# Kernel optimization log

Hardware: AMD Instinct MI355X
Metric: run time of the kernel (lower is better)

## Reference

```python
import jax, jax.numpy as jnp
import numpy as np

EPS = 1e-7
N, L, BATCH = 512, 2, 128
N_IPF = 10


def setup_inputs() -> dict:
    key = jax.random.key(0)
    k1, k2, k3, k4 = jax.random.split(key, 4)
    return {
        "x": jax.random.randint(k1, (BATCH, N), 0, L, dtype=jnp.int32),
        "W": jax.random.normal(k2, (N, N), dtype=jnp.float32),
        "V_compress": jax.random.normal(k3, (N, L), dtype=jnp.float32),
        "E_compress": jax.random.normal(k4, (N, N, L, L), dtype=jnp.float32),
    }


def _moat_forward(W, V_compress, E_compress, x):
    n, l = V_compress.shape
    # marginals / joints
    V = jax.nn.softmax(V_compress, axis=1)              # (n, l)
    E = jnp.exp(E_compress)                              # (n, n, l, l)
    E = E / E.sum(axis=(-2, -1), keepdims=True)

    # 10-step Sinkhorn / IPF projection onto marginals V
    A_b = V[:, None, :, None]                            # (n, 1, l, 1)
    B_b = V[None, :, None, :]                            # (1, n, 1, l)
    for _ in range(N_IPF):
        row_marg = E.sum(axis=3, keepdims=True) + EPS    # (n, n, l, 1)
        col_marg = E.sum(axis=2, keepdims=True) + EPS    # (n, n, 1, l)
        E = E * (A_b / row_marg)
        E = E * (B_b / col_marg)
        E = E / (E.sum(axis=(-2, -1), keepdims=True) + EPS)

    # zero the diagonal (i == j) pairwise joints, clamp
    E = E * (1.0 - jnp.eye(n, dtype=E.dtype))[:, :, None, None]
    E = jnp.clip(E, 0.0, 1.0)

    # symmetric edge-weight matrix from strictly-lower-triangular sigmoid(W)
    Wm = jax.nn.sigmoid(W)
    Wm = jnp.tril(Wm, k=-1)
    Wm = Wm.T + Wm                                       # (n, n), zero diag
    L_0 = -Wm + jnp.diag(Wm.sum(axis=1))                 # graph Laplacian

    idx = jnp.arange(n)
    # Pr[b, i] = V[i, x[b, i]]
    Pr = V[idx[None, :], x]                              # (batch, n)
    # P[b, i, j] = E[i, j, x[b, i], x[b, j]]
    P = E[idx[None, :, None], idx[None, None, :], x[:, :, None], x[:, None, :]]  # (batch, n, n)
    P = P / (Pr[:, :, None] * Pr[:, None, :])

    WP = Wm[None, :, :] * P                              # (batch, n, n)
    Lb = -WP + jax.vmap(jnp.diag)(WP.sum(axis=2))        # batched Laplacian

    # matrix-tree theorem: logdet of the (n-1, n-1) principal minor
    _, logdet_L = jnp.linalg.slogdet(Lb[:, 1:, 1:])
    _, logdet_L0 = jnp.linalg.slogdet(L_0[1:, 1:])
    return jnp.log(Pr).sum(axis=1) + logdet_L - logdet_L0  # (batch,)


def reference(x, W, V_compress, E_compress):
    return _moat_forward(W, V_compress, E_compress, x)
```

## Files before the change

### kernel.cpp

```cpp
#include <hip/hip_runtime.h>
#include <hip/hip_bf16.h>
#include <math.h>

#define NDIM 512
#define NB   128
#define NMAT 129
#define EPSF 1e-7f
#define MS  ((size_t)262144)
#define LTS ((size_t)32768)
#define PSTR ((size_t)524288)

#define OFF_E   ((size_t)0)
#define OFF_WM  ((size_t)1048576)
#define OFF_V   ((size_t)(OFF_WM + 262144))
#define OFF_IPR ((size_t)(OFF_V + 1024))
#define OFF_LPR ((size_t)(OFF_IPR + 65536))
#define OFF_LD  ((size_t)(OFF_LPR + 128))
#define OFF_LT  ((size_t)1377792)
#define OFF_MAT ((size_t)(OFF_LT + (size_t)NMAT*LTS))

__device__ __forceinline__ float rdlane(float v, int l) {
  return __uint_as_float((unsigned)__builtin_amdgcn_readlane((int)__float_as_uint(v), l));
}

__global__ __launch_bounds__(256) void k_V(const float* __restrict__ Vc, float* __restrict__ V) {
  int i = blockIdx.x * 256 + threadIdx.x;
  if (i < NDIM) {
    float v0 = Vc[2*i], v1 = Vc[2*i+1];
    float mx = fmaxf(v0, v1);
    float e0 = expf(v0 - mx), e1 = expf(v1 - mx);
    float s = e0 + e1;
    V[2*i]   = e0 / s;
    V[2*i+1] = e1 / s;
  }
}

__global__ __launch_bounds__(256) void k_Wm(const float* __restrict__ W, float* __restrict__ Wm) {
  int idx = blockIdx.x * 256 + threadIdx.x;
  int i = idx >> 9, j = idx & 511;
  float v = 0.f;
  if (i > j)      v = 1.f / (1.f + expf(-W[i*NDIM + j]));
  else if (i < j) v = 1.f / (1.f + expf(-W[j*NDIM + i]));
  Wm[idx] = v;
}

__global__ __launch_bounds__(256) void k_E(const float* __restrict__ Ec, const float* __restrict__ V,
                                           float* __restrict__ E2) {
  int idx = blockIdx.x * 256 + threadIdx.x;
  int i = idx >> 9, j = idx & 511;
  float4 ec = reinterpret_cast<const float4*>(Ec)[idx];
  float e00 = expf(ec.x), e01 = expf(ec.y), e10 = expf(ec.z), e11 = expf(ec.w);
  float s = e00 + e01 + e10 + e11;
  float inv = 1.f / s;
  e00 *= inv; e01 *= inv; e10 *= inv; e11 *= inv;
  float A0 = V[2*i], A1 = V[2*i+1];
  float B0 = V[2*j], B1 = V[2*j+1];
  for (int t = 0; t < 10; ++t) {
    float rm0 = e00 + e01 + EPSF, rm1 = e10 + e11 + EPSF;
    float cm0 = e00 + e10 + EPSF, cm1 = e01 + e11 + EPSF;
    float f0 = A0 / rm0, f1 = A1 / rm1;
    e00 *= f0; e01 *= f0; e10 *= f1; e11 *= f1;
    float g0 = B0 / cm0, g1 = B1 / cm1;
    e00 *= g0; e10 *= g0; e01 *= g1; e11 *= g1;
    float ss = e00 + e01 + e10 + e11 + EPSF;
    float iv = 1.f / ss;
    e00 *= iv; e01 *= iv; e10 *= iv; e11 *= iv;
  }
  if (i == j) { e00 = 0.f; e01 = 0.f; e10 = 0.f; e11 = 0.f; }
  e00 = fminf(fmaxf(e00, 0.f), 1.f);
  e01 = fminf(fmaxf(e01, 0.f), 1.f);
  e10 = fminf(fmaxf(e10, 0.f), 1.f);
  e11 = fminf(fmaxf(e11, 0.f), 1.f);
  reinterpret_cast<float2*>(E2)[idx]               = make_float2(e00, e01);
  reinterpret_cast<float2*>(E2 + PSTR)[idx]        = make_float2(e10, e11);
}

__global__ __launch_bounds__(256) void k_Pr(const int* __restrict__ x, const float* __restrict__ V,
                                            float* __restrict__ invPr, float* __restrict__ logPr) {
  const int b = blockIdx.x;
  const int tid = threadIdx.x;
  float acc = 0.f;
  for (int ii = tid; ii < NDIM; ii += 256) {
    const int xv = x[b*NDIM + ii];
    const float p = V[2*ii + xv];
    invPr[b*NDIM + ii] = 1.f / p;
    acc += logf(p);
  }
  for (int off = 32; off > 0; off >>= 1) acc += __shfl_down(acc, off, 64);
  __shared__ float sw[4];
  if ((tid & 63) == 0) sw[tid >> 6] = acc;
  __syncthreads();
  if (tid == 0) logPr[b] = sw[0] + sw[1] + sw[2] + sw[3];
}

__global__ __launch_bounds__(512) void k_build(const int* __restrict__ x, const float* __restrict__ E2,
                                               const float* __restrict__ Wm, const float* __restrict__ invPr,
                                               float* __restrict__ Mall) {
  const int b = blockIdx.x;
  const int i = blockIdx.y*8 + (threadIdx.x >> 6);
  const int lane = threadIdx.x & 63;
  const int j0 = lane << 3;

  const float4 w0 = *(const float4*)(Wm + (size_t)i*NDIM + j0);
  const float4 w1 = *(const float4*)(Wm + (size_t)i*NDIM + j0 + 4);
  float wp[8];
  if (b < NB) {
    const int   xi   = x[b*NDIM + i];
    const float ipri = invPr[b*NDIM + i];
    const int4  xa = *(const int4*)(x + b*NDIM + j0);
    const int4  xb = *(const int4*)(x + b*NDIM + j0 + 4);
    const float4 pa = *(const float4*)(invPr + b*NDIM + j0);
    const float4 pb = *(const float4*)(invPr + b*NDIM + j0 + 4);
    const float* pl = E2 + (size_t)xi*PSTR + ((size_t)i*NDIM + j0)*2;
    const float4 ea = *(const float4*)(pl);
    const float4 eb = *(const float4*)(pl + 4);
    const float4 ec = *(const float4*)(pl + 8);
    const float4 ed = *(const float4*)(pl + 12);
    wp[0] = w0.x * (xa.x ? ea.y : ea.x) * pa.x;
    wp[1] = w0.y * (xa.y ? ea.w : ea.z) * pa.y;
    wp[2] = w0.z * (xa.z ? eb.y : eb.x) * pa.z;
    wp[3] = w0.w * (xa.w ? eb.w : eb.z) * pa.w;
    wp[4] = w1.x * (xb.x ? ec.y : ec.x) * pb.x;
    wp[5] = w1.y * (xb.y ? ec.w : ec.z) * pb.y;
    wp[6] = w1.z * (xb.z ? ed.y : ed.x) * pb.z;
    wp[7] = w1.w * (xb.w ? ed.w : ed.z) * pb.w;
    #pragma unroll
    for (int k = 0; k < 8; ++k) wp[k] *= ipri;
  } else {
    wp[0]=w0.x; wp[1]=w0.y; wp[2]=w0.z; wp[3]=w0.w;
    wp[4]=w1.x; wp[5]=w1.y; wp[6]=w1.z; wp[7]=w1.w;
  }
  float s = ((wp[0]+wp[1])+(wp[2]+wp[3])) + ((wp[4]+wp[5])+(wp[6]+wp[7]));
  #pragma unroll
  for (int off = 32; off > 0; off >>= 1) s += __shfl_xor(s, off, 64);

  float o[8];
  #pragma unroll
  for (int k = 0; k < 8; ++k) o[k] = -wp[k];
  if (i == 0) {
    #pragma unroll
    for (int k = 0; k < 8; ++k) o[k] = 0.f;
    if (lane == 0) o[0] = 1.f;
  } else {
    if (lane == 0) o[0] = 0.f;
    #pragma unroll
    for (int k = 0; k < 8; ++k)
      if (j0 + k == i) o[k] = s;
  }
  float* dst = Mall + (size_t)b*MS + (size_t)i*NDIM + j0;
  *(float4*)(dst)   = make_float4(o[0],o[1],o[2],o[3]);
  *(float4*)(dst+4) = make_float4(o[4],o[5],o[6],o[7]);
}

template<int KK>
struct WFact {
  static __device__ __forceinline__ void run(float (&a)[64], const int lane,
                                             float& mypiv, float& myrec) {
    const float piv = rdlane(a[KK], KK);
    const float rec = 1.0f / piv;
    if (lane == KK) { mypiv = piv; myrec = rec; }
    if (lane > KK) {
      const float l = a[KK] * rec;
      a[KK] = l;
      #pragma unroll
      for (int c = KK + 1; c < 64; ++c)
        a[c] -= l * rdlane(a[c], KK);
    }
    WFact<KK + 1>::run(a, lane, mypiv, myrec);
  }
};
template<>
struct WFact<64> {
  static __device__ __forceinline__ void run(float (&)[64], int, float&, float&) {}
};

template<int C>
struct SolveStep {
  static __device__ __forceinline__ void run(float (&a)[64], const float (*T)[72]) {
    float acc = a[C];
    #pragma unroll
    for (int p = 0; p < C; ++p)
      acc -= a[p] * T[C][p];
    a[C] = acc * T[C][66];
    SolveStep<C + 1>::run(a, T);
  }
};
template<>
struct SolveStep<64> {
  static __device__ __forceinline__ void run(float (&)[64], const float (*)[72]) {}
};

__global__ __launch_bounds__(512) void k_panel(float* __restrict__ Mall, float* __restrict__ Lt,
                                               float* __restrict__ logdets, int k0, int mrem) {
  const int b = blockIdx.x;
  float* __restrict__ M = Mall + (size_t)b*MS;
  float* __restrict__ L = Lt + (size_t)b*LTS;
  const int t = threadIdx.x;
  const int m = NDIM - k0;
  __shared__ float T[64][72];

  float a[64];
  if (t < m) {
    const float* row = M + (size_t)(k0+t)*NDIM + k0;
    #pragma unroll
    for (int c4 = 0; c4 < 16; ++c4) {
      float4 v = *(const float4*)(row + c4*4);
      a[c4*4+0]=v.x; a[c4*4+1]=v.y; a[c4*4+2]=v.z; a[c4*4+3]=v.w;
    }
  }

  if (t < 64) {
    float mypiv = 1.f, myrec = 1.f;
    WFact<0>::run(a, t, mypiv, myrec);
    #pragma unroll
    for (int c = 0; c < 64; ++c) T[c][t] = a[c];
    T[t][66] = myrec;
    float v = logf(fabsf(mypiv));
    #pragma unroll
    for (int off = 32; off > 0; off >>= 1) v += __shfl_down(v, off, 64);
    if (t == 0) logdets[b] = (k0 == 0) ? v : (logdets[b] + v);
  }
  __syncthreads();

  if (mrem > 0) {
    if (t >= 64 && t < m) {
      SolveStep<0>::run(a, T);
      #pragma unroll
      for (int c = 0; c < 64; ++c) L[(size_t)c*NDIM + t] = a[c];
    }
    if (t < mrem) {
      const int col = k0 + 64 + t;
      float u[64];
      #pragma unroll
      for (int r = 0; r < 64; ++r) u[r] = M[(size_t)(k0+r)*NDIM + col];
      #pragma unroll
      for (int p = 0; p < 63; ++p) {
        const float lv = u[p];
        #pragma unroll
        for (int kk = p+1; kk < 64; ++kk)
          u[kk] -= T[p][kk] * lv;
      }
      #pragma unroll
      for (int r = 1; r < 64; ++r) M[(size_t)(k0+r)*NDIM + col] = u[r];
    }
  }
}

__global__ __launch_bounds__(256, 4) void k_gemm(float* __restrict__ Mall, const float* __restrict__ Lt,
                                                 int k0) {
  const int b = blockIdx.x;
  float* __restrict__ M = Mall + (size_t)b*MS;
  const float* __restrict__ L = Lt + (size_t)b*LTS;
  __shared__ float As[64][68];
  __shared__ float Bs[64][68];
  const int tid = threadIdx.x;
  const int tx = tid & 15, ty = tid >> 4;
  const int rowbase = 64 + blockIdx.y*64;
  const int colbase = 64 + blockIdx.z*64;
  #pragma unroll
  for (int i = 0; i < 4; ++i) {
    int q = tid + 256*i;
    int p = q >> 4, f = q & 15;
    *(float4*)&As[p][f*4] = *(const float4*)&L[(size_t)p*NDIM + rowbase + f*4];
    *(float4*)&Bs[p][f*4] = *(const float4*)&M[(size_t)(k0+p)*NDIM + (k0+colbase) + f*4];
  }
  float* Crow = M + (size_t)(k0+rowbase+ty*4)*NDIM + (k0+colbase+tx*4);
  float4 c0 = *(float4*)(Crow + 0*NDIM);
  float4 c1 = *(float4*)(Crow + 1*NDIM);
  float4 c2 = *(float4*)(Crow + 2*NDIM);
  float4 c3 = *(float4*)(Crow + 3*NDIM);
  __syncthreads();
  #pragma unroll
  for (int p = 0; p < 64; ++p) {
    const float4 av = *(const float4*)&As[p][ty*4];
    const float4 bv = *(const float4*)&Bs[p][tx*4];
    c0.x -= av.x*bv.x; c0.y -= av.x*bv.y; c0.z -= av.x*bv.z; c0.w -= av.x*bv.w;
    c1.x -= av.y*bv.x; c1.y -= av.y*bv.y; c1.z -= av.y*bv.z; c1.w -= av.y*bv.w;
    c2.x -= av.z*bv.x; c2.y -= av.z*bv.y; c2.z -= av.z*bv.z; c2.w -= av.z*bv.w;
    c3.x -= av.w*bv.x; c3.y -= av.w*bv.y; c3.z -= av.w*bv.z; c3.w -= av.w*bv.w;
  }
  *(float4*)(Crow + 0*NDIM) = c0;
  *(float4*)(Crow + 1*NDIM) = c1;
  *(float4*)(Crow + 2*NDIM) = c2;
  *(float4*)(Crow + 3*NDIM) = c3;
}

__global__ void k_final(const float* __restrict__ logPr, const float* __restrict__ logdets,
                        float* __restrict__ out) {
  int t = threadIdx.x;
  if (t < NB) out[t] = logPr[t] + logdets[t] - logdets[NB];
}

extern "C" void kernel_launch(void* const* d_in, const int* in_sizes, int n_in,
                              void* d_out, int out_size, void* d_ws, size_t ws_size,
                              hipStream_t stream) {
  const int*   x  = (const int*)  d_in[0];
  const float* W  = (const float*)d_in[1];
  const float* Vc = (const float*)d_in[2];
  const float* Ec = (const float*)d_in[3];
  float* out = (float*)d_out;
  float* ws  = (float*)d_ws;
  (void)in_sizes; (void)n_in; (void)out_size; (void)ws_size;

  float* Mat = ws + OFF_MAT;
  float* Lt  = ws + OFF_LT;
  float* Ld  = ws + OFF_LD;

  k_V  <<<2,    256, 0, stream>>>(Vc, ws + OFF_V);
  k_Wm <<<1024, 256, 0, stream>>>(W,  ws + OFF_WM);
  k_E  <<<1024, 256, 0, stream>>>(Ec, ws + OFF_V, ws + OFF_E);
  k_Pr <<<NB,   256, 0, stream>>>(x,  ws + OFF_V, ws + OFF_IPR, ws + OFF_LPR);
  dim3 gb(NMAT, 64);
  k_build<<<gb, 512, 0, stream>>>(x, ws + OFF_E, ws + OFF_WM, ws + OFF_IPR, Mat);

  for (int s = 0; s < 8; ++s) {
    const int k0 = s*64;
    const int mrem = NDIM - k0 - 64;
    k_panel<<<NMAT, 512, 0, stream>>>(Mat, Lt, Ld, k0, mrem);
    if (mrem > 0) {
      const int nt = mrem/64;
      dim3 gg(NMAT, nt, nt);
      k_gemm<<<gg, 256, 0, stream>>>(Mat, Lt, k0);
    }
  }
  k_final<<<1, 128, 0, stream>>>(ws + OFF_LPR, Ld, out);
}
```

Measured before the change: 628.1 us.

## Switch blocked LU to 128-wide panels and fuse prep kernels

The blocked LU factorization now processes 128-column panels in four steps instead of 64-column panels in eight. Each panel kernel factors two 64-wide sub-blocks in shared memory, and the trailing GEMM does a rank-128 update that reads L directly from the matrix rather than from a separate Lt buffer. This halves the number of panel/GEMM launch pairs and the global round-trips of the trailing matrix. The softmax, sigmoid and Sinkhorn prep kernels are merged into one, with V recomputed inline in k_Pr. In exchange, the panel kernel does much more serial work per block and uses more registers, which may lengthen its critical path.

Result: slower. 1.003 ms (+59.8%).

```diff
diff --git a/kernel.cpp b/kernel.cpp
--- a/kernel.cpp
+++ b/kernel.cpp
@@ -7,54 +7,43 @@
 #define NMAT 129
 #define EPSF 1e-7f
 #define MS  ((size_t)262144)
-#define LTS ((size_t)32768)
 #define PSTR ((size_t)524288)
 
 #define OFF_E   ((size_t)0)
 #define OFF_WM  ((size_t)1048576)
-#define OFF_V   ((size_t)(OFF_WM + 262144))
-#define OFF_IPR ((size_t)(OFF_V + 1024))
-#define OFF_LPR ((size_t)(OFF_IPR + 65536))
-#define OFF_LD  ((size_t)(OFF_LPR + 128))
-#define OFF_LT  ((size_t)1377792)
-#define OFF_MAT ((size_t)(OFF_LT + (size_t)NMAT*LTS))
+#define OFF_IPR ((size_t)1310720)
+#define OFF_LPR ((size_t)1376256)
+#define OFF_LD  ((size_t)1376384)
+#define OFF_MAT ((size_t)1377792)
 
 __device__ __forceinline__ float rdlane(float v, int l) {
   return __uint_as_float((unsigned)__builtin_amdgcn_readlane((int)__float_as_uint(v), l));
 }
 
-__global__ __launch_bounds__(256) void k_V(const float* __restrict__ Vc, float* __restrict__ V) {
-  int i = blockIdx.x * 256 + threadIdx.x;
-  if (i < NDIM) {
-    float v0 = Vc[2*i], v1 = Vc[2*i+1];
-    float mx = fmaxf(v0, v1);
-    float e0 = expf(v0 - mx), e1 = expf(v1 - mx);
-    float s = e0 + e1;
-    V[2*i]   = e0 / s;
-    V[2*i+1] = e1 / s;
-  }
-}
-
-__global__ __launch_bounds__(256) void k_Wm(const float* __restrict__ W, float* __restrict__ Wm) {
+__global__ __launch_bounds__(256) void k_prep(const float* __restrict__ W, const float* __restrict__ Vc,
+                                              const float* __restrict__ Ec, float* __restrict__ Wm,
+                                              float* __restrict__ E2) {
   int idx = blockIdx.x * 256 + threadIdx.x;
   int i = idx >> 9, j = idx & 511;
-  float v = 0.f;
-  if (i > j)      v = 1.f / (1.f + expf(-W[i*NDIM + j]));
-  else if (i < j) v = 1.f / (1.f + expf(-W[j*NDIM + i]));
-  Wm[idx] = v;
-}
-
-__global__ __launch_bounds__(256) void k_E(const float* __restrict__ Ec, const float* __restrict__ V,
-                                           float* __restrict__ E2) {
-  int idx = blockIdx.x * 256 + threadIdx.x;
-  int i = idx >> 9, j = idx & 511;
+  float wv = 0.f;
+  if (i > j)      wv = 1.f / (1.f + expf(-W[i*NDIM + j]));
+  else if (i < j) wv = 1.f / (1.f + expf(-W[j*NDIM + i]));
+  Wm[idx] = wv;
+  float vi0 = Vc[2*i], vi1 = Vc[2*i+1];
+  float mi = fmaxf(vi0, vi1);
+  float ei0 = expf(vi0 - mi), ei1 = expf(vi1 - mi);
+  float si = ei0 + ei1;
+  float A0 = ei0 / si, A1 = ei1 / si;
+  float vj0 = Vc[2*j], vj1 = Vc[2*j+1];
+  float mj = fmaxf(vj0, vj1);
+  float ej0 = expf(vj0 - mj), ej1 = expf(vj1 - mj);
+  float sj = ej0 + ej1;
+  float B0 = ej0 / sj, B1 = ej1 / sj;
   float4 ec = reinterpret_cast<const float4*>(Ec)[idx];
   float e00 = expf(ec.x), e01 = expf(ec.y), e10 = expf(ec.z), e11 = expf(ec.w);
   float s = e00 + e01 + e10 + e11;
   float inv = 1.f / s;
   e00 *= inv; e01 *= inv; e10 *= inv; e11 *= inv;
-  float A0 = V[2*i], A1 = V[2*i+1];
-  float B0 = V[2*j], B1 = V[2*j+1];
   for (int t = 0; t < 10; ++t) {
     float rm0 = e00 + e01 + EPSF, rm1 = e10 + e11 + EPSF;
     float cm0 = e00 + e10 + EPSF, cm1 = e01 + e11 + EPSF;
@@ -71,18 +60,22 @@
   e01 = fminf(fmaxf(e01, 0.f), 1.f);
   e10 = fminf(fmaxf(e10, 0.f), 1.f);
   e11 = fminf(fmaxf(e11, 0.f), 1.f);
-  reinterpret_cast<float2*>(E2)[idx]               = make_float2(e00, e01);
-  reinterpret_cast<float2*>(E2 + PSTR)[idx]        = make_float2(e10, e11);
-}
-
-__global__ __launch_bounds__(256) void k_Pr(const int* __restrict__ x, const float* __restrict__ V,
+  reinterpret_cast<float2*>(E2)[idx]        = make_float2(e00, e01);
+  reinterpret_cast<float2*>(E2 + PSTR)[idx] = make_float2(e10, e11);
+}
+
+__global__ __launch_bounds__(256) void k_Pr(const int* __restrict__ x, const float* __restrict__ Vc,
                                             float* __restrict__ invPr, float* __restrict__ logPr) {
   const int b = blockIdx.x;
   const int tid = threadIdx.x;
   float acc = 0.f;
   for (int ii = tid; ii < NDIM; ii += 256) {
     const int xv = x[b*NDIM + ii];
-    const float p = V[2*ii + xv];
+    float v0 = Vc[2*ii], v1 = Vc[2*ii+1];
+    float mx = fmaxf(v0, v1);
+    float e0 = expf(v0 - mx), e1 = expf(v1 - mx);
+    float s = e0 + e1;
+    const float p = xv ? (e1 / s) : (e0 / s);
     invPr[b*NDIM + ii] = 1.f / p;
     acc += logf(p);
   }
@@ -176,7 +169,7 @@
 
 template<int C>
 struct SolveStep {
-  static __device__ __forceinline__ void run(float (&a)[64], const float (*T)[72]) {
+  static __device__ __forceinline__ void run(float (&a)[64], const float (*T)[68]) {
     float acc = a[C];
     #pragma unroll
     for (int p = 0; p < C; ++p)
@@ -187,19 +180,22 @@
 };
 template<>
 struct SolveStep<64> {
-  static __device__ __forceinline__ void run(float (&)[64], const float (*)[72]) {}
+  static __device__ __forceinline__ void run(float (&)[64], const float (*)[68]) {}
 };
 
-__global__ __launch_bounds__(512) void k_panel(float* __restrict__ Mall, float* __restrict__ Lt,
-                                               float* __restrict__ logdets, int k0, int mrem) {
+__global__ __launch_bounds__(512) void k_panel128(float* __restrict__ Mall,
+                                                  float* __restrict__ logdets, int k0, int ncols) {
   const int b = blockIdx.x;
   float* __restrict__ M = Mall + (size_t)b*MS;
-  float* __restrict__ L = Lt + (size_t)b*LTS;
   const int t = threadIdx.x;
   const int m = NDIM - k0;
-  __shared__ float T[64][72];
+  __shared__ float T0[64][68];
+  __shared__ float TU[64][68];
+  __shared__ float Ls2[64][68];
+  __shared__ float red[2];
 
   float a[64];
+  float strip[64];
   if (t < m) {
     const float* row = M + (size_t)(k0+t)*NDIM + k0;
     #pragma unroll
@@ -207,68 +203,168 @@
       float4 v = *(const float4*)(row + c4*4);
       a[c4*4+0]=v.x; a[c4*4+1]=v.y; a[c4*4+2]=v.z; a[c4*4+3]=v.w;
     }
+    if (t >= 64) {
+      #pragma unroll
+      for (int c4 = 0; c4 < 16; ++c4) {
+        float4 v = *(const float4*)(row + 64 + c4*4);
+        strip[c4*4+0]=v.x; strip[c4*4+1]=v.y; strip[c4*4+2]=v.z; strip[c4*4+3]=v.w;
+      }
+    }
   }
 
   if (t < 64) {
     float mypiv = 1.f, myrec = 1.f;
     WFact<0>::run(a, t, mypiv, myrec);
     #pragma unroll
-    for (int c = 0; c < 64; ++c) T[c][t] = a[c];
-    T[t][66] = myrec;
+    for (int c = 0; c < 64; ++c) T0[c][t] = a[c];
+    T0[t][66] = myrec;
     float v = logf(fabsf(mypiv));
     #pragma unroll
     for (int off = 32; off > 0; off >>= 1) v += __shfl_down(v, off, 64);
-    if (t == 0) logdets[b] = (k0 == 0) ? v : (logdets[b] + v);
-  }
-  __syncthreads();
-
-  if (mrem > 0) {
-    if (t >= 64 && t < m) {
-      SolveStep<0>::run(a, T);
-      #pragma unroll
-      for (int c = 0; c < 64; ++c) L[(size_t)c*NDIM + t] = a[c];
-    }
-    if (t < mrem) {
-      const int col = k0 + 64 + t;
-      float u[64];
-      #pragma unroll
-      for (int r = 0; r < 64; ++r) u[r] = M[(size_t)(k0+r)*NDIM + col];
-      #pragma unroll
-      for (int p = 0; p < 63; ++p) {
-        const float lv = u[p];
-        #pragma unroll
-        for (int kk = p+1; kk < 64; ++kk)
-          u[kk] -= T[p][kk] * lv;
-      }
-      #pragma unroll
-      for (int r = 1; r < 64; ++r) M[(size_t)(k0+r)*NDIM + col] = u[r];
-    }
-  }
-}
-
-__global__ __launch_bounds__(256, 4) void k_gemm(float* __restrict__ Mall, const float* __restrict__ Lt,
-                                                 int k0) {
+    if (t == 0) red[0] = v;
+  }
+  __syncthreads();
+
+  if (t >= 64 && t < m) {
+    SolveStep<0>::run(a, T0);
+    if (t < 128) {
+      #pragma unroll
+      for (int c = 0; c < 64; ++c) Ls2[c][t-64] = a[c];
+    }
+  }
+  if (t < 64) {
+    const int col = k0 + 64 + t;
+    float u[64];
+    #pragma unroll
+    for (int r = 0; r < 64; ++r) u[r] = M[(size_t)(k0+r)*NDIM + col];
+    #pragma unroll
+    for (int p = 0; p < 63; ++p) {
+      const float lv = u[p];
+      #pragma unroll
+      for (int kk = p+1; kk < 64; ++kk) u[kk] -= T0[p][kk] * lv;
+    }
+    #pragma unroll
+    for (int r = 0; r < 64; ++r) TU[r][t] = u[r];
+  }
+  __syncthreads();
+
+  if (t >= 64 && t < m) {
+    #pragma unroll
+    for (int p = 0; p < 64; ++p) {
+      const float lv = a[p];
+      #pragma unroll
+      for (int c = 0; c < 64; ++c) strip[c] -= TU[p][c] * lv;
+    }
+  }
+  __syncthreads();
+
+  if (t >= 64 && t < 128) {
+    float mypiv = 1.f, myrec = 1.f;
+    WFact<0>::run(strip, t & 63, mypiv, myrec);
+    #pragma unroll
+    for (int c = 0; c < 64; ++c) TU[c][t-64] = strip[c];
+    TU[t-64][66] = myrec;
+    float v = logf(fabsf(mypiv));
+    #pragma unroll
+    for (int off = 32; off > 0; off >>= 1) v += __shfl_down(v, off, 64);
+    if (t == 64) red[1] = v;
+  }
+  __syncthreads();
+
+  if (t >= 128 && t < m) SolveStep<0>::run(strip, TU);
+
+  if (t >= 128 && t < m) {
+    float* row = M + (size_t)(k0+t)*NDIM + k0;
+    #pragma unroll
+    for (int c4 = 0; c4 < 16; ++c4)
+      *(float4*)(row + c4*4) = make_float4(a[c4*4],a[c4*4+1],a[c4*4+2],a[c4*4+3]);
+    #pragma unroll
+    for (int c4 = 0; c4 < 16; ++c4)
+      *(float4*)(row + 64 + c4*4) = make_float4(strip[c4*4],strip[c4*4+1],strip[c4*4+2],strip[c4*4+3]);
+  }
+
+  if (t < ncols) {
+    const int col = k0 + 128 + t;
+    float u0[64], u1[64];
+    #pragma unroll
+    for (int r = 0; r < 64; ++r) u0[r] = M[(size_t)(k0+r)*NDIM + col];
+    #pragma unroll
+    for (int r = 0; r < 64; ++r) u1[r] = M[(size_t)(k0+64+r)*NDIM + col];
+    #pragma unroll
+    for (int p = 0; p < 63; ++p) {
+      const float lv = u0[p];
+      #pragma unroll
+      for (int kk = p+1; kk < 64; ++kk) u0[kk] -= T0[p][kk] * lv;
+    }
+    #pragma unroll
+    for (int p = 0; p < 64; ++p) {
+      const float lv = u0[p];
+      #pragma unroll
+      for (int r = 0; r < 64; ++r) u1[r] -= Ls2[p][r] * lv;
+    }
+    #pragma unroll
+    for (int p = 0; p < 63; ++p) {
+      const float lv = u1[p];
+      #pragma unroll
+      for (int kk = p+1; kk < 64; ++kk) u1[kk] -= TU[p][kk] * lv;
+    }
+    #pragma unroll
+    for (int r = 1; r < 64; ++r) M[(size_t)(k0+r)*NDIM + col] = u0[r];
+    #pragma unroll
+    for (int r = 0; r < 64; ++r) M[(size_t)(k0+64+r)*NDIM + col] = u1[r];
+  }
+
+  if (t == 0) {
+    float v = red[0] + red[1];
+    logdets[b] = (k0 == 0) ? v : (logdets[b] + v);
+  }
+}
+
+__global__ __launch_bounds__(256, 4) void k_gemm2(float* __restrict__ Mall, int k0) {
   const int b = blockIdx.x;
   float* __restrict__ M = Mall + (size_t)b*MS;
-  const float* __restrict__ L = Lt + (size_t)b*LTS;
   __shared__ float As[64][68];
   __shared__ float Bs[64][68];
   const int tid = threadIdx.x;
   const int tx = tid & 15, ty = tid >> 4;
-  const int rowbase = 64 + blockIdx.y*64;
-  const int colbase = 64 + blockIdx.z*64;
-  #pragma unroll
-  for (int i = 0; i < 4; ++i) {
-    int q = tid + 256*i;
-    int p = q >> 4, f = q & 15;
-    *(float4*)&As[p][f*4] = *(const float4*)&L[(size_t)p*NDIM + rowbase + f*4];
-    *(float4*)&Bs[p][f*4] = *(const float4*)&M[(size_t)(k0+p)*NDIM + (k0+colbase) + f*4];
-  }
+  const int rowbase = 128 + blockIdx.y*64;
+  const int colbase = 128 + blockIdx.z*64;
   float* Crow = M + (size_t)(k0+rowbase+ty*4)*NDIM + (k0+colbase+tx*4);
   float4 c0 = *(float4*)(Crow + 0*NDIM);
   float4 c1 = *(float4*)(Crow + 1*NDIM);
   float4 c2 = *(float4*)(Crow + 2*NDIM);
   float4 c3 = *(float4*)(Crow + 3*NDIM);
+  #pragma unroll
+  for (int i = 0; i < 4; ++i) {
+    const int q = tid + 256*i, qr = q >> 4, qf = q & 15;
+    const float4 va = *(const float4*)&M[(size_t)(k0+rowbase+qr)*NDIM + k0 + qf*4];
+    As[qf*4+0][qr]=va.x; As[qf*4+1][qr]=va.y; As[qf*4+2][qr]=va.z; As[qf*4+3][qr]=va.w;
+    *(float4*)&Bs[qr][qf*4] = *(const float4*)&M[(size_t)(k0+qr)*NDIM + (k0+colbase) + qf*4];
+  }
+  __syncthreads();
+  float4 ra[4], rb[4];
+  #pragma unroll
+  for (int i = 0; i < 4; ++i) {
+    const int q = tid + 256*i, qr = q >> 4, qf = q & 15;
+    ra[i] = *(const float4*)&M[(size_t)(k0+rowbase+qr)*NDIM + k0 + 64 + qf*4];
+    rb[i] = *(const float4*)&M[(size_t)(k0+64+qr)*NDIM + (k0+colbase) + qf*4];
+  }
+  #pragma unroll
+  for (int p = 0; p < 64; ++p) {
+    const float4 av = *(const float4*)&As[p][ty*4];
+    const float4 bv = *(const float4*)&Bs[p][tx*4];
+    c0.x -= av.x*bv.x; c0.y -= av.x*bv.y; c0.z -= av.x*bv.z; c0.w -= av.x*bv.w;
+    c1.x -= av.y*bv.x; c1.y -= av.y*bv.y; c1.z -= av.y*bv.z; c1.w -= av.y*bv.w;
+    c2.x -= av.z*bv.x; c2.y -= av.z*bv.y; c2.z -= av.z*bv.z; c2.w -= av.z*bv.w;
+    c3.x -= av.w*bv.x; c3.y -= av.w*bv.y; c3.z -= av.w*bv.z; c3.w -= av.w*bv.w;
+  }
+  __syncthreads();
+  #pragma unroll
+  for (int i = 0; i < 4; ++i) {
+    const int q = tid + 256*i, qr = q >> 4, qf = q & 15;
+    As[qf*4+0][qr]=ra[i].x; As[qf*4+1][qr]=ra[i].y; As[qf*4+2][qr]=ra[i].z; As[qf*4+3][qr]=ra[i].w;
+    *(float4*)&Bs[qr][qf*4] = rb[i];
+  }
   __syncthreads();
   #pragma unroll
   for (int p = 0; p < 64; ++p) {
@@ -303,24 +399,21 @@
   (void)in_sizes; (void)n_in; (void)out_size; (void)ws_size;
 
   float* Mat = ws + OFF_MAT;
-  float* Lt  = ws + OFF_LT;
   float* Ld  = ws + OFF_LD;
 
-  k_V  <<<2,    256, 0, stream>>>(Vc, ws + OFF_V);
-  k_Wm <<<1024, 256, 0, stream>>>(W,  ws + OFF_WM);
-  k_E  <<<1024, 256, 0, stream>>>(Ec, ws + OFF_V, ws + OFF_E);
-  k_Pr <<<NB,   256, 0, stream>>>(x,  ws + OFF_V, ws + OFF_IPR, ws + OFF_LPR);
+  k_prep<<<1024, 256, 0, stream>>>(W, Vc, Ec, ws + OFF_WM, ws + OFF_E);
+  k_Pr  <<<NB,   256, 0, stream>>>(x, Vc, ws + OFF_IPR, ws + OFF_LPR);
   dim3 gb(NMAT, 64);
   k_build<<<gb, 512, 0, stream>>>(x, ws + OFF_E, ws + OFF_WM, ws + OFF_IPR, Mat);
 
-  for (int s = 0; s < 8; ++s) {
-    const int k0 = s*64;
-    const int mrem = NDIM - k0 - 64;
-    k_panel<<<NMAT, 512, 0, stream>>>(Mat, Lt, Ld, k0, mrem);
-    if (mrem > 0) {
-      const int nt = mrem/64;
+  for (int S = 0; S < 4; ++S) {
+    const int k0 = S*128;
+    const int ncols = NDIM - k0 - 128;
+    k_panel128<<<NMAT, 512, 0, stream>>>(Mat, Ld, k0, ncols);
+    if (ncols > 0) {
+      const int nt = ncols/64;
       dim3 gg(NMAT, nt, nt);
-      k_gemm<<<gg, 256, 0, stream>>>(Mat, Lt, k0);
+      k_gemm2<<<gg, 256, 0, stream>>>(Mat, k0);
     }
   }
   k_final<<<1, 128, 0, stream>>>(ws + OFF_LPR, Ld, out);
```
